# Optimization experiments

Hardware: AMD Instinct MI355X
Metric: run time of the kernel (lower is better)

## Reference

```python
import jax, jax.numpy as jnp
import numpy as np

EMBED = 1024
HEADS = 16
HEAD_DIM = EMBED // HEADS
B, S = 2, 2048


def setup_inputs() -> dict:
    key = jax.random.key(0)
    ks = jax.random.split(key, 11)
    sc = 1.0 / np.sqrt(EMBED)
    d = {
        'query': jax.random.normal(ks[0], (B, S, EMBED), jnp.float32),
        'key':   jax.random.normal(ks[1], (B, S, EMBED), jnp.float32),
        'value': jax.random.normal(ks[2], (B, S, EMBED), jnp.float32),
        'Wq': jax.random.normal(ks[3], (EMBED, EMBED), jnp.float32) * sc,
        'bq': jnp.zeros((EMBED,), jnp.float32),
        'Wk': jax.random.normal(ks[4], (EMBED, EMBED), jnp.float32) * sc,
        'bk': jnp.zeros((EMBED,), jnp.float32),
        'Wv': jax.random.normal(ks[5], (EMBED, EMBED), jnp.float32) * sc,
        'bv': jnp.zeros((EMBED,), jnp.float32),
        'Wo': jax.random.normal(ks[6], (EMBED, EMBED), jnp.float32) * sc,
        'bo': jnp.zeros((EMBED,), jnp.float32),
    }
    return d


def _split_heads(x):
    b, s, _ = x.shape
    return x.reshape(b, s, HEADS, HEAD_DIM).transpose(0, 2, 1, 3)  # [B,H,S,D]


def reference(query, key, value, Wq, bq, Wk, bk, Wv, bv, Wo, bo):
    # nn.Linear: y = x @ W^T + b
    q = _split_heads(query @ Wq.T + bq)
    k = _split_heads(key @ Wk.T + bk)
    v = _split_heads(value @ Wv.T + bv)
    scale = 1.0 / np.sqrt(HEAD_DIM).astype(np.float32)
    attn = jnp.einsum('bhqd,bhkd->bhqk', q, k) * scale  # [B,H,S,S]
    attn = jax.nn.softmax(attn, axis=-1)
    out = jnp.einsum('bhqk,bhkd->bhqd', attn, v)
    out = out.transpose(0, 2, 1, 3).reshape(query.shape[0], -1, EMBED)
    return out @ Wo.T + bo
```

## Files before the change

### kernel.cpp

```cpp
#include <hip/hip_runtime.h>

typedef _Float16 f16;
typedef __fp16   fp16n2 __attribute__((ext_vector_type(2)));
typedef _Float16 f16x8 __attribute__((ext_vector_type(8)));
typedef float    f32x2 __attribute__((ext_vector_type(2)));
typedef float    f32x4 __attribute__((ext_vector_type(4)));
typedef float    f32x16 __attribute__((ext_vector_type(16)));
typedef int      i32x2 __attribute__((ext_vector_type(2)));
typedef unsigned short u16;
typedef unsigned long long u64;

#define B_ 2
#define S_ 2048
#define E_ 1024
#define H_ 16
#define D_ 64
#define M_ (B_*S_)
#define LOG2E 1.44269504088896340736f

__device__ __forceinline__ f32x4 mfma16(f16x8 a, f16x8 b, f32x4 c) {
  return __builtin_amdgcn_mfma_f32_16x16x32_f16(a, b, c, 0, 0, 0);
}
__device__ __forceinline__ f32x16 mfma32(f16x8 a, f16x8 b, f32x16 c) {
  return __builtin_amdgcn_mfma_f32_32x32x16_f16(a, b, c, 0, 0, 0);
}

__device__ __forceinline__ void gload_lds16(const void* g, void* l) {
  __builtin_amdgcn_global_load_lds(
      (const __attribute__((address_space(1))) unsigned int*)g,
      (__attribute__((address_space(3))) unsigned int*)l, 16, 0, 0);
}

__device__ __forceinline__ int pkrtz(float a, float b) {
  union { fp16n2 h; int i; } u;
  u.h = __builtin_amdgcn_cvt_pkrtz(a, b);
  return u.i;
}

__device__ __forceinline__ u16 f16bits(float x) {
  union { f16 h; u16 u; } c; c.h = (f16)x; return c.u;
}

__device__ __forceinline__ f32x16 Z16() {
  f32x16 z = {0.f,0.f,0.f,0.f,0.f,0.f,0.f,0.f,0.f,0.f,0.f,0.f,0.f,0.f,0.f,0.f};
  return z;
}

__device__ __forceinline__ f32x2 pr2(const f32x16& v, int j) {
  return (f32x2){v[2 * j], v[2 * j + 1]};
}

__global__ __launch_bounds__(256) void cast_all(
    const float* __restrict__ q, const float* __restrict__ k, const float* __restrict__ v,
    const float* __restrict__ wq, const float* __restrict__ wk,
    const float* __restrict__ wv, const float* __restrict__ wo,
    f16* __restrict__ xq, f16* __restrict__ xk, f16* __restrict__ xv,
    f16* __restrict__ wqh, f16* __restrict__ wkh, f16* __restrict__ wvh,
    f16* __restrict__ woh) {
  int i = blockIdx.x * 256 + threadIdx.x;
  const float* src; f16* dst; int off;
  if (i < 3 * 524288) {
    int seg = i >> 19; off = i & 524287;
    src = seg == 0 ? q : seg == 1 ? k : v;
    dst = seg == 0 ? xq : seg == 1 ? xk : xv;
  } else {
    int j = i - 3 * 524288;
    int seg = j >> 17; off = j & 131071;
    src = seg == 0 ? wq : seg == 1 ? wk : seg == 2 ? wv : wo;
    dst = seg == 0 ? wqh : seg == 1 ? wkh : seg == 2 ? wvh : woh;
  }
  const float4* s = (const float4*)src;
  float4 a = s[off * 2], b = s[off * 2 + 1];
  f16x8 o = { (f16)a.x, (f16)a.y, (f16)a.z, (f16)a.w,
              (f16)b.x, (f16)b.y, (f16)b.z, (f16)b.w };
  *(f16x8*)&dst[(size_t)off * 8] = o;
}

__device__ __forceinline__ void gemm_core128(const f16* __restrict__ A,
                                             const f16* __restrict__ Bm,
                                             int m0, int n0,
                                             f32x4 (&acc)[4][2]) {
  __shared__ f16 Al[2][128 * 32];
  __shared__ f16 Bl[2][128 * 32];
  const int tid = threadIdx.x;
  const int w = tid >> 6, lane = tid & 63, lg = lane >> 4, ll = lane & 15;
  const int wr = (w & 1) * 64, wc = (w >> 1) * 32;

  const f32x4 zero4 = {0.f, 0.f, 0.f, 0.f};
#pragma unroll
  for (int m = 0; m < 4; ++m) { acc[m][0] = zero4; acc[m][1] = zero4; }

  const int lgs = (lg ^ ((ll >> 1) & 3)) * 8;
  const int row = tid >> 2;
  const int c8  = ((tid & 3) ^ ((tid >> 3) & 3)) * 8;

  for (int k0 = 0; k0 < 1024; k0 += 64) {
    __syncthreads();
#pragma unroll
    for (int ks = 0; ks < 2; ++ks) {
      gload_lds16(&A [(size_t)(m0 + row) * 1024 + k0 + ks * 32 + c8], &Al[ks][tid * 8]);
      gload_lds16(&Bm[(size_t)(n0 + row) * 1024 + k0 + ks * 32 + c8], &Bl[ks][tid * 8]);
    }
    __syncthreads();

#pragma unroll
    for (int ks = 0; ks < 2; ++ks) {
      f16x8 af[4], bf[2];
#pragma unroll
      for (int m = 0; m < 4; ++m) af[m] = *(const f16x8*)&Al[ks][(wr + m * 16 + ll) * 32 + lgs];
#pragma unroll
      for (int n = 0; n < 2; ++n) bf[n] = *(const f16x8*)&Bl[ks][(wc + n * 16 + ll) * 32 + lgs];
#pragma unroll
      for (int m = 0; m < 4; ++m)
#pragma unroll
        for (int n = 0; n < 2; ++n) acc[m][n] = mfma16(af[m], bf[n], acc[m][n]);
    }
  }
}

__global__ __launch_bounds__(512, 4) void gemm_qkv(
    const f16* __restrict__ Xq, const f16* __restrict__ Xk, const f16* __restrict__ Xv,
    const f16* __restrict__ Wq, const f16* __restrict__ Wk, const f16* __restrict__ Wv,
    const float* __restrict__ bq, const float* __restrict__ bk, const float* __restrict__ bv,
    f16* __restrict__ Qb, f16* __restrict__ Kb, f16* __restrict__ Vt) {
  const int z = blockIdx.z;
  const f16*   A    = (z == 0) ? Xq : (z == 1) ? Xk : Xv;
  const f16*   Bm   = (z == 0) ? Wq : (z == 1) ? Wk : Wv;
  const float* bias = (z == 0) ? bq : (z == 1) ? bk : bv;
  const float scale = (z == 0) ? (0.125f * LOG2E) : 1.0f;
  const int m0 = blockIdx.x * 128, n0 = blockIdx.y * 128;

  f32x4 acc[4][2];
  gemm_core128(A, Bm, m0, n0, acc);

  const int tid = threadIdx.x;
  const int w = tid >> 6, lane = tid & 63, lg = lane >> 4, ll = lane & 15;
  const int wr = (w & 1) * 64, wc = (w >> 1) * 32;

  if (z == 2) {
#pragma unroll
    for (int m = 0; m < 4; ++m)
#pragma unroll
      for (int n = 0; n < 2; ++n) {
        int col = n0 + wc + n * 16 + ll;
        float bv_ = bias[col];
        int h = col >> 6, d = col & 63;
        int rowb = m0 + wr + m * 16 + lg * 4;
        int b = rowb >> 11, s = rowb & 2047;
        u64 pk = (u64)f16bits(acc[m][n][0] + bv_)
               | ((u64)f16bits(acc[m][n][1] + bv_) << 16)
               | ((u64)f16bits(acc[m][n][2] + bv_) << 32)
               | ((u64)f16bits(acc[m][n][3] + bv_) << 48);
        *(u64*)&Vt[(((size_t)(b * H_ + h)) * D_ + d) * S_ + s] = pk;
      }
    return;
  }

  f16* dst = (z == 0) ? Qb : Kb;
#pragma unroll
  for (int m = 0; m < 4; ++m)
#pragma unroll
    for (int n = 0; n < 2; ++n) {
      int col = n0 + wc + n * 16 + ll;
      float bv_ = bias[col];
      int h = col >> 6, d = col & 63;
#pragma unroll
      for (int r = 0; r < 4; ++r) {
        int row = m0 + wr + m * 16 + lg * 4 + r;
        int b = row >> 11, s = row & 2047;
        float v = (acc[m][n][r] + bv_) * scale;
        dst[(((size_t)(b * H_ + h)) * S_ + s) * D_ + d] = (f16)v;
      }
    }
}

__device__ __forceinline__ void gemm_core64(const f16* __restrict__ A,
                                            const f16* __restrict__ Bm,
                                            int m0, int n0,
                                            f32x4 (&acc)[4][2]) {
  __shared__ f16 Al[2][128 * 32];
  __shared__ f16 Bl[2][64 * 32];
  const int tid = threadIdx.x;
  const int w = tid >> 6, lane = tid & 63, lg = lane >> 4, ll = lane & 15;
  const int wr = (w >> 1) * 64, wc = (w & 1) * 32;

  const f32x4 zero4 = {0.f, 0.f, 0.f, 0.f};
#pragma unroll
  for (int m = 0; m < 4; ++m) { acc[m][0] = zero4; acc[m][1] = zero4; }

  const int lgs = (lg ^ ((ll >> 1) & 3)) * 8;

  for (int k0 = 0; k0 < 1024; k0 += 64) {
    __syncthreads();
#pragma unroll
    for (int ks = 0; ks < 2; ++ks) {
#pragma unroll
      for (int it = 0; it < 2; ++it) {
        int chunk = it * 256 + tid;
        int row = chunk >> 2;
        int c8 = ((chunk & 3) ^ ((chunk >> 3) & 3)) * 8;
        gload_lds16(&A[(size_t)(m0 + row) * 1024 + k0 + ks * 32 + c8],
                    &Al[ks][chunk * 8]);
      }
      {
        int chunk = tid;
        int row = chunk >> 2;
        int c8 = ((chunk & 3) ^ ((chunk >> 3) & 3)) * 8;
        gload_lds16(&Bm[(size_t)(n0 + row) * 1024 + k0 + ks * 32 + c8],
                    &Bl[ks][chunk * 8]);
      }
    }
    __syncthreads();

#pragma unroll
    for (int ks = 0; ks < 2; ++ks) {
      f16x8 af[4], bf[2];
#pragma unroll
      for (int m = 0; m < 4; ++m) af[m] = *(const f16x8*)&Al[ks][(wr + m * 16 + ll) * 32 + lgs];
#pragma unroll
      for (int n = 0; n < 2; ++n) bf[n] = *(const f16x8*)&Bl[ks][(wc + n * 16 + ll) * 32 + lgs];
#pragma unroll
      for (int m = 0; m < 4; ++m)
#pragma unroll
        for (int n = 0; n < 2; ++n) acc[m][n] = mfma16(af[m], bf[n], acc[m][n]);
    }
  }
}

__global__ __launch_bounds__(256) void gemm_out(const f16* __restrict__ A,
                                                const f16* __restrict__ W,
                                                const float* __restrict__ bias,
                                                float* __restrict__ out) {
  const int m0 = blockIdx.x * 128, n0 = blockIdx.y * 64;
  f32x4 acc[4][2];
  gemm_core64(A, W, m0, n0, acc);

  const int tid = threadIdx.x;
  const int w = tid >> 6, lane = tid & 63, lg = lane >> 4, ll = lane & 15;
  const int wr = (w >> 1) * 64, wc = (w & 1) * 32;
#pragma unroll
  for (int m = 0; m < 4; ++m)
#pragma unroll
    for (int n = 0; n < 2; ++n) {
      int col = n0 + wc + n * 16 + ll;
      float bv_ = bias[col];
#pragma unroll
      for (int r = 0; r < 4; ++r) {
        int row = m0 + wr + m * 16 + lg * 4 + r;
        out[(size_t)row * 1024 + col] = acc[m][n][r] + bv_;
      }
    }
}

__global__ __launch_bounds__(512, 4) void attn_fwd(const f16* __restrict__ Q,
                                                   const f16* __restrict__ K,
                                                   const f16* __restrict__ VT,
                                                   f16* __restrict__ O) {
  const int qt = blockIdx.x, bh = blockIdx.y;
  const int tid = threadIdx.x;
  const int w = tid >> 6, lane = tid & 63;
  const int ql = lane & 31, hi = lane >> 5;
  const int qsub = w & 3, kvh = w >> 2;

  __shared__ __align__(16) char smem[65536];
  char* hbase = smem + kvh * 32768;

  const f16* Qb = Q  + (size_t)bh * S_ * D_;
  const f16* Kb = K  + (size_t)bh * S_ * D_ + (size_t)(kvh * 1024) * D_;
  const f16* Vb = VT + (size_t)bh * D_ * S_ + kvh * 1024;
  const int q0 = qt * 128 + qsub * 32;

  f16x8 qf[4];
#pragma unroll
  for (int ks = 0; ks < 4; ++ks)
    qf[ks] = *(const f16x8*)&Qb[(size_t)(q0 + ql) * 64 + ks * 16 + hi * 8];

  f32x16 accO[2];
  accO[0] = Z16(); accO[1] = Z16();
  float l_r = 0.f;

  const int seg = w & 3;
  const int lr = lane >> 3;
  const int lc = lane & 7;
  const int cs = lc ^ lr;

#define STAGE(kt_)                                                             \
  {                                                                            \
    char* Kl_ = hbase + ((kt_) & 1) * 16384;                                   \
    char* Vl_ = Kl_ + 8192;                                                    \
    _Pragma("unroll")                                                          \
    for (int i_ = 0; i_ < 2; ++i_) {                                           \
      int r_ = seg * 16 + i_ * 8 + lr;                                         \
      gload_lds16(&Kb[(size_t)((kt_) * 64 + r_) * 64 + cs * 8],                \
                  Kl_ + seg * 2048 + i_ * 1024);                               \
      gload_lds16(&Vb[(size_t)r_ * S_ + (kt_) * 64 + cs * 8],                  \
                  Vl_ + seg * 2048 + i_ * 1024);                               \
    }                                                                          \
  }

  STAGE(0);

#pragma unroll 1
  for (int kt = 0; kt < 16; ++kt) {
    __syncthreads();
    if (kt + 1 < 16) STAGE(kt + 1);

    char* KlB = hbase + (kt & 1) * 16384;
    char* VlB = KlB + 8192;

    f32x16 accS[2];
    __builtin_amdgcn_s_setprio(1);
#pragma unroll
    for (int c = 0; c < 2; ++c) {
      int row = c * 32 + ql;
      int rb = row * 128, sw = (row & 7) << 4;
      f16x8 kf0 = *(const f16x8*)(KlB + rb + ((hi * 16) ^ sw));
      accS[c] = mfma32(kf0, qf[0], Z16());
#pragma unroll
      for (int ks = 1; ks < 4; ++ks) {
        f16x8 kf = *(const f16x8*)(KlB + rb + (((ks * 2 + hi) * 16) ^ sw));
        accS[c] = mfma32(kf, qf[ks], accS[c]);
      }
    }
    __builtin_amdgcn_s_setprio(0);

    f32x2 rs2 = {0.f, 0.f};
#pragma unroll
    for (int c = 0; c < 2; ++c)
#pragma unroll
      for (int j = 0; j < 8; ++j) {
        float p0 = __builtin_amdgcn_exp2f(accS[c][2 * j]);
        float p1 = __builtin_amdgcn_exp2f(accS[c][2 * j + 1]);
        accS[c][2 * j]     = p0;
        accS[c][2 * j + 1] = p1;
        rs2 += (f32x2){p0, p1};
      }
    l_r += rs2.x + rs2.y;

#pragma unroll
    for (int c = 0; c < 2; ++c)
#pragma unroll
      for (int s = 0; s < 2; ++s) {
        int b0 = s * 8;
        int a0 = pkrtz(accS[c][b0 + 0], accS[c][b0 + 1]);
        int a1 = pkrtz(accS[c][b0 + 2], accS[c][b0 + 3]);
        int a2 = pkrtz(accS[c][b0 + 4], accS[c][b0 + 5]);
        int a3 = pkrtz(accS[c][b0 + 6], accS[c][b0 + 7]);
        i32x2 r02 = __builtin_amdgcn_permlane32_swap(a0, a2, false, false);
        i32x2 r13 = __builtin_amdgcn_permlane32_swap(a1, a3, false, false);
        union { int i[4]; f16x8 h; } pf;
        pf.i[0] = r02.x; pf.i[1] = r13.x; pf.i[2] = r02.y; pf.i[3] = r13.y;
        int kvb = c * 64 + s * 32 + hi * 16;
        __builtin_amdgcn_s_setprio(1);
#pragma unroll
        for (int dc = 0; dc < 2; ++dc) {
          int dr = dc * 32 + ql;
          f16x8 vf = *(const f16x8*)(VlB + dr * 128 + (kvb ^ ((dr & 7) << 4)));
          accO[dc] = mfma32(vf, pf.h, accO[dc]);
        }
        __builtin_amdgcn_s_setprio(0);
      }
  }
#undef STAGE

  l_r += __shfl_xor(l_r, 32);

  __syncthreads();
  float* lB = (float*)smem;
  if (kvh == 1) {
    if (hi == 0) lB[qsub * 32 + ql] = l_r;
#pragma unroll
    for (int dc = 0; dc < 2; ++dc)
#pragma unroll
      for (int g = 0; g < 4; ++g) {
        int d0 = g * 8 + hi * 4 + dc * 32;
        f32x4 v = { accO[dc][g * 4 + 0], accO[dc][g * 4 + 1],
                    accO[dc][g * 4 + 2], accO[dc][g * 4 + 3] };
        *(f32x4*)(smem + 32768 + qsub * 8192 + ql * 256 + ((d0 * 4) ^ ((ql & 7) << 4))) = v;
      }
  }
  __syncthreads();
  f16* Ep = (f16*)(smem + 1024);
  if (kvh == 0) {
    float inv = 1.0f / (l_r + lB[qsub * 32 + ql]);
#pragma unroll
    for (int dc = 0; dc < 2; ++dc)
#pragma unroll
      for (int g = 0; g < 4; ++g) {
        int d0 = g * 8 + hi * 4 + dc * 32;
        f32x4 o2 = *(const f32x4*)(smem + 32768 + qsub * 8192 + ql * 256 +
                                   ((d0 * 4) ^ ((ql & 7) << 4)));
        u64 pk = (u64)f16bits((accO[dc][g * 4 + 0] + o2[0]) * inv)
               | ((u64)f16bits((accO[dc][g * 4 + 1] + o2[1]) * inv) << 16)
               | ((u64)f16bits((accO[dc][g * 4 + 2] + o2[2]) * inv) << 32)
               | ((u64)f16bits((accO[dc][g * 4 + 3] + o2[3]) * inv) << 48);
        *(u64*)&Ep[(qsub * 32 + ql) * 68 + d0] = pk;
      }
  }
  __syncthreads();
  const int b = bh >> 4, h = bh & 15;
#pragma unroll
  for (int pass = 0; pass < 2; ++pass) {
    int idx = pass * 512 + tid;
    int row = idx >> 3, cx = idx & 7;
    f16x8 v = *(const f16x8*)&Ep[row * 68 + cx * 8];
    *(f16x8*)&O[((size_t)(b * S_ + qt * 128 + row)) * E_ + h * 64 + cx * 8] = v;
  }
}

extern "C" void kernel_launch(void* const* d_in, const int* in_sizes, int n_in,
                              void* d_out, int out_size, void* d_ws, size_t ws_size,
                              hipStream_t stream) {
  (void)in_sizes; (void)n_in; (void)out_size; (void)ws_size;
  const float* q  = (const float*)d_in[0];
  const float* k  = (const float*)d_in[1];
  const float* v  = (const float*)d_in[2];
  const float* Wq = (const float*)d_in[3];
  const float* bq = (const float*)d_in[4];
  const float* Wk = (const float*)d_in[5];
  const float* bk = (const float*)d_in[6];
  const float* Wv = (const float*)d_in[7];
  const float* bv = (const float*)d_in[8];
  const float* Wo = (const float*)d_in[9];
  const float* bo = (const float*)d_in[10];
  float* out = (float*)d_out;

  f16* ws  = (f16*)d_ws;
  f16* Xq  = ws;
  f16* Xk  = Xq  + (size_t)M_ * E_;
  f16* Xv  = Xk  + (size_t)M_ * E_;
  f16* Wqh = Xv  + (size_t)M_ * E_;
  f16* Wkh = Wqh + (size_t)E_ * E_;
  f16* Wvh = Wkh + (size_t)E_ * E_;
  f16* Woh = Wvh + (size_t)E_ * E_;
  f16* Qb  = Woh + (size_t)E_ * E_;
  f16* Kb  = Qb  + (size_t)M_ * E_;
  f16* VTb = Kb  + (size_t)M_ * E_;
  f16* AO  = Xq;

  cast_all<<<8192, 256, 0, stream>>>(q, k, v, Wq, Wk, Wv, Wo,
                                     Xq, Xk, Xv, Wqh, Wkh, Wvh, Woh);

  gemm_qkv<<<dim3(M_ / 128, E_ / 128, 3), 512, 0, stream>>>(
      Xq, Xk, Xv, Wqh, Wkh, Wvh, bq, bk, bv, Qb, Kb, VTb);

  attn_fwd<<<dim3(S_ / 128, B_ * H_), 512, 0, stream>>>(Qb, Kb, VTb, AO);

  gemm_out<<<dim3(M_ / 128, E_ / 64), 256, 0, stream>>>(AO, Woh, bo, out);
}
```

Baseline: 113.8 us.

## Halve attention LDS to single-buffered KV and fp16 merge scratch for occupancy

Cuts the attention kernel's shared memory from 64KB to 32KB. It drops the K/V double buffer for a single buffer loaded between two barriers, and exchanges the partial output of the second KV half in fp16 within the epilogue buffer instead of a separate fp32 region. Launch bounds rise to 8 blocks per SM to allow more resident waves. In exchange, global loads no longer overlap with MFMA compute inside a block, and the cross-half merge loses some precision.

```diff
diff --git a/kernel.cpp b/kernel.cpp
--- a/kernel.cpp
+++ b/kernel.cpp
@@ -252,7 +252,7 @@
     }
 }
 
-__global__ __launch_bounds__(512, 4) void attn_fwd(const f16* __restrict__ Q,
+__global__ __launch_bounds__(512, 8) void attn_fwd(const f16* __restrict__ Q,
                                                    const f16* __restrict__ K,
                                                    const f16* __restrict__ VT,
                                                    f16* __restrict__ O) {
@@ -262,8 +262,8 @@
   const int ql = lane & 31, hi = lane >> 5;
   const int qsub = w & 3, kvh = w >> 2;
 
-  __shared__ __align__(16) char smem[65536];
-  char* hbase = smem + kvh * 32768;
+  __shared__ __align__(16) char smem[32768];
+  char* hb = smem + kvh * 16384;
 
   const f16* Qb = Q  + (size_t)bh * S_ * D_;
   const f16* Kb = K  + (size_t)bh * S_ * D_ + (size_t)(kvh * 1024) * D_;
@@ -284,29 +284,21 @@
   const int lc = lane & 7;
   const int cs = lc ^ lr;
 
-#define STAGE(kt_)                                                             \
-  {                                                                            \
-    char* Kl_ = hbase + ((kt_) & 1) * 16384;                                   \
-    char* Vl_ = Kl_ + 8192;                                                    \
-    _Pragma("unroll")                                                          \
-    for (int i_ = 0; i_ < 2; ++i_) {                                           \
-      int r_ = seg * 16 + i_ * 8 + lr;                                         \
-      gload_lds16(&Kb[(size_t)((kt_) * 64 + r_) * 64 + cs * 8],                \
-                  Kl_ + seg * 2048 + i_ * 1024);                               \
-      gload_lds16(&Vb[(size_t)r_ * S_ + (kt_) * 64 + cs * 8],                  \
-                  Vl_ + seg * 2048 + i_ * 1024);                               \
-    }                                                                          \
-  }
-
-  STAGE(0);
-
 #pragma unroll 1
   for (int kt = 0; kt < 16; ++kt) {
     __syncthreads();
-    if (kt + 1 < 16) STAGE(kt + 1);
-
-    char* KlB = hbase + (kt & 1) * 16384;
-    char* VlB = KlB + 8192;
+#pragma unroll
+    for (int i_ = 0; i_ < 2; ++i_) {
+      int r_ = seg * 16 + i_ * 8 + lr;
+      gload_lds16(&Kb[(size_t)(kt * 64 + r_) * 64 + cs * 8],
+                  hb + seg * 2048 + i_ * 1024);
+      gload_lds16(&Vb[(size_t)r_ * S_ + kt * 64 + cs * 8],
+                  hb + 8192 + seg * 2048 + i_ * 1024);
+    }
+    __syncthreads();
+
+    char* KlB = hb;
+    char* VlB = hb + 8192;
 
     f32x16 accS[2];
     __builtin_amdgcn_s_setprio(1);
@@ -361,12 +353,12 @@
         __builtin_amdgcn_s_setprio(0);
       }
   }
-#undef STAGE
 
   l_r += __shfl_xor(l_r, 32);
 
   __syncthreads();
   float* lB = (float*)smem;
+  f16* Ep = (f16*)(smem + 1024);
   if (kvh == 1) {
     if (hi == 0) lB[qsub * 32 + ql] = l_r;
 #pragma unroll
@@ -374,13 +366,14 @@
 #pragma unroll
       for (int g = 0; g < 4; ++g) {
         int d0 = g * 8 + hi * 4 + dc * 32;
-        f32x4 v = { accO[dc][g * 4 + 0], accO[dc][g * 4 + 1],
-                    accO[dc][g * 4 + 2], accO[dc][g * 4 + 3] };
-        *(f32x4*)(smem + 32768 + qsub * 8192 + ql * 256 + ((d0 * 4) ^ ((ql & 7) << 4))) = v;
+        u64 pk = (u64)f16bits(accO[dc][g * 4 + 0])
+               | ((u64)f16bits(accO[dc][g * 4 + 1]) << 16)
+               | ((u64)f16bits(accO[dc][g * 4 + 2]) << 32)
+               | ((u64)f16bits(accO[dc][g * 4 + 3]) << 48);
+        *(u64*)&Ep[(qsub * 32 + ql) * 68 + d0] = pk;
       }
   }
   __syncthreads();
-  f16* Ep = (f16*)(smem + 1024);
   if (kvh == 0) {
     float inv = 1.0f / (l_r + lB[qsub * 32 + ql]);
 #pragma unroll
@@ -388,12 +381,12 @@
 #pragma unroll
       for (int g = 0; g < 4; ++g) {
         int d0 = g * 8 + hi * 4 + dc * 32;
-        f32x4 o2 = *(const f32x4*)(smem + 32768 + qsub * 8192 + ql * 256 +
-                                   ((d0 * 4) ^ ((ql & 7) << 4)));
-        u64 pk = (u64)f16bits((accO[dc][g * 4 + 0] + o2[0]) * inv)
-               | ((u64)f16bits((accO[dc][g * 4 + 1] + o2[1]) * inv) << 16)
-               | ((u64)f16bits((accO[dc][g * 4 + 2] + o2[2]) * inv) << 32)
-               | ((u64)f16bits((accO[dc][g * 4 + 3] + o2[3]) * inv) << 48);
+        union { u64 v; f16 h[4]; } o2;
+        o2.v = *(const u64*)&Ep[(qsub * 32 + ql) * 68 + d0];
+        u64 pk = (u64)f16bits((accO[dc][g * 4 + 0] + (float)o2.h[0]) * inv)
+               | ((u64)f16bits((accO[dc][g * 4 + 1] + (float)o2.h[1]) * inv) << 16)
+               | ((u64)f16bits((accO[dc][g * 4 + 2] + (float)o2.h[2]) * inv) << 32)
+               | ((u64)f16bits((accO[dc][g * 4 + 3] + (float)o2.h[3]) * inv) << 48);
         *(u64*)&Ep[(qsub * 32 + ql) * 68 + d0] = pk;
       }
   }
```

Result: slower. 399.7 us (+251.2%).
